# Kernel optimization log

Hardware: AMD Instinct MI355X
Metric: run time of the kernel (lower is better)

## Reference

```python
import jax, jax.numpy as jnp
import numpy as np

B, S, D, H, DK = 2, 2048, 1024, 16, 64  # d_model = n_heads * d_k

def setup_inputs() -> dict:
    key = jax.random.key(0)
    ks = jax.random.split(key, 11)
    s = 1.0 / np.sqrt(D)
    return {
        "Q": jax.random.normal(ks[0], (B, S, D), jnp.float32),
        "K": jax.random.normal(ks[1], (B, S, D), jnp.float32),
        "V": jax.random.normal(ks[2], (B, S, D), jnp.float32),
        "wq": jax.random.normal(ks[3], (D, D), jnp.float32) * s,
        "bq": jnp.zeros((D,), jnp.float32),
        "wk": jax.random.normal(ks[4], (D, D), jnp.float32) * s,
        "bk": jnp.zeros((D,), jnp.float32),
        "wv": jax.random.normal(ks[5], (D, D), jnp.float32) * s,
        "bv": jnp.zeros((D,), jnp.float32),
        "wo": jax.random.normal(ks[6], (D, D), jnp.float32) * s,
        "bo": jnp.zeros((D,), jnp.float32),
    }

def reference(Q, K, V, wq, bq, wk, bk, wv, bv, wo, bo):
    # linear projections (torch Linear: x @ W^T + b)
    q = Q @ wq.T + bq
    k = K @ wk.T + bk
    v = V @ wv.T + bv
    # split heads -> [B, H, S, DK]
    def split(t):
        return t.reshape(B, S, H, DK).transpose(0, 2, 1, 3)
    q, k, v = split(q), split(k), split(v)
    scale = 1.0 / np.sqrt(DK)
    scores = jnp.einsum('bhqd,bhkd->bhqk', q, k) * scale  # [B,H,S,S]
    probs = jax.nn.softmax(scores, axis=-1)
    # dropout is identity in eval mode
    ctx = jnp.einsum('bhqk,bhkd->bhqd', probs, v)  # [B,H,S,DK]
    ctx = ctx.transpose(0, 2, 1, 3).reshape(B, S, D)
    return ctx @ wo.T + bo
```

## Files before the change

kernel.cpp:

```cpp
#include <hip/hip_runtime.h>

#define S_LEN 2048
#define DMODEL 1024
#define DHEAD 64

typedef _Float16 half8 __attribute__((ext_vector_type(8)));
typedef _Float16 half4 __attribute__((ext_vector_type(4)));
typedef float f32x4 __attribute__((ext_vector_type(4)));

#define LOG2E 1.4426950408889634f

__device__ __forceinline__ void async_copy16(const void* g, void* l) {
  __builtin_amdgcn_global_load_lds((__attribute__((address_space(1))) const void*)g,
                                   (__attribute__((address_space(3))) void*)l,
                                   16, 0, 0);
}

__device__ __forceinline__ void stage16_cvt(const float* __restrict__ gp, _Float16* lp) {
  float4 f0 = ((const float4*)gp)[0];
  float4 f1 = ((const float4*)gp)[1];
  float4 f2 = ((const float4*)gp)[2];
  float4 f3 = ((const float4*)gp)[3];
  half8 h0, h1;
  h0[0] = (_Float16)f0.x; h0[1] = (_Float16)f0.y; h0[2] = (_Float16)f0.z; h0[3] = (_Float16)f0.w;
  h0[4] = (_Float16)f1.x; h0[5] = (_Float16)f1.y; h0[6] = (_Float16)f1.z; h0[7] = (_Float16)f1.w;
  h1[0] = (_Float16)f2.x; h1[1] = (_Float16)f2.y; h1[2] = (_Float16)f2.z; h1[3] = (_Float16)f2.w;
  h1[4] = (_Float16)f3.x; h1[5] = (_Float16)f3.y; h1[6] = (_Float16)f3.z; h1[7] = (_Float16)f3.w;
  *(half8*)lp = h0;
  *(half8*)(lp + 8) = h1;
}

__global__ __launch_bounds__(256) void convert_w(const float* __restrict__ wq,
                                                 const float* __restrict__ wk,
                                                 const float* __restrict__ wv,
                                                 _Float16* __restrict__ dst) {
  const float* src = (blockIdx.y == 0) ? wq : (blockIdx.y == 1) ? wk : wv;
  _Float16* d = dst + (size_t)blockIdx.y * (DMODEL * DMODEL);
  int i = (blockIdx.x * 256 + threadIdx.x) * 4;
  float4 v = *(const float4*)(src + i);
  half4 h;
  h[0] = (_Float16)v.x; h[1] = (_Float16)v.y;
  h[2] = (_Float16)v.z; h[3] = (_Float16)v.w;
  *(half4*)(d + i) = h;
}

__global__ __launch_bounds__(256) void convert_wo(const float* __restrict__ wo,
                                                  _Float16* __restrict__ dst) {
  int i = (blockIdx.x * 256 + threadIdx.x) * 4;
  float4 v = *(const float4*)(wo + i);
  half4 h;
  h[0] = (_Float16)v.x; h[1] = (_Float16)v.y;
  h[2] = (_Float16)v.z; h[3] = (_Float16)v.w;
  *(half4*)(dst + i) = h;
}

__global__ __launch_bounds__(256) void qkv_gemm(
    const float* __restrict__ Qf, const float* __restrict__ Kf, const float* __restrict__ Vf,
    const _Float16* __restrict__ wh,
    const float* __restrict__ bq, const float* __restrict__ bk, const float* __restrict__ bv,
    _Float16* __restrict__ qo, _Float16* __restrict__ ko, _Float16* __restrict__ vt) {
  __shared__ __align__(16) _Float16 As[128 * 32];
  __shared__ __align__(16) _Float16 Bs[128 * 32];
  const int tid = threadIdx.x;
  const int wave = tid >> 6, lane = tid & 63;
  const int m15 = lane & 15, quad = lane >> 4;
  const int m0 = blockIdx.x * 128;
  const int gn0 = blockIdx.y * 128;
  const int sel = gn0 >> 10;
  const int n0 = gn0 & 1023;
  const float* Ag = (sel == 0) ? Qf : (sel == 1) ? Kf : Vf;
  const _Float16* Wg = wh + (size_t)sel * (DMODEL * DMODEL);
  const float* bias = (sel == 0) ? bq : (sel == 1) ? bk : bv;

  const int wm = (wave & 1) * 64, wn = (wave >> 1) * 64;
  const int sr = tid >> 1, sc16 = (tid & 1) * 16;

  f32x4 acc[4][4];
#pragma unroll
  for (int i = 0; i < 4; i++)
#pragma unroll
    for (int j = 0; j < 4; j++) {
      f32x4 z = {0.f, 0.f, 0.f, 0.f};
      acc[i][j] = z;
    }

  for (int k0 = 0; k0 < DMODEL; k0 += 32) {
#pragma unroll
    for (int p = 0; p < 2; p++) {
      int e = p * 2048 + tid * 8;
      async_copy16(Wg + (size_t)(n0 + (e >> 5)) * DMODEL + k0 + (e & 31),
                   (char*)Bs + p * 4096 + wave * 1024);
    }
    stage16_cvt(Ag + (size_t)(m0 + sr) * DMODEL + k0 + sc16, &As[sr * 32 + sc16]);
    __syncthreads();
    half8 af[4], bf[4];
#pragma unroll
    for (int i = 0; i < 4; i++)
      af[i] = *(const half8*)&As[(wm + i * 16 + m15) * 32 + quad * 8];
#pragma unroll
    for (int j = 0; j < 4; j++)
      bf[j] = *(const half8*)&Bs[(wn + j * 16 + m15) * 32 + quad * 8];
#pragma unroll
    for (int i = 0; i < 4; i++)
#pragma unroll
      for (int j = 0; j < 4; j++)
        acc[i][j] = __builtin_amdgcn_mfma_f32_16x16x32_f16(af[i], bf[j], acc[i][j], 0, 0, 0);
    __syncthreads();
  }
  if (sel != 2) {
    _Float16* outp = (sel == 0) ? qo : ko;
    const float scale = (sel == 0) ? (0.125f * LOG2E) : 1.0f;
#pragma unroll
    for (int i = 0; i < 4; i++) {
#pragma unroll
      for (int j = 0; j < 4; j++) {
        int gn = n0 + wn + j * 16 + m15;
        float bb = bias[gn];
#pragma unroll
        for (int r = 0; r < 4; r++) {
          int gm = m0 + wm + i * 16 + quad * 4 + r;
          outp[(size_t)gm * DMODEL + gn] = (_Float16)((acc[i][j][r] + bb) * scale);
        }
      }
    }
  } else {
#pragma unroll
    for (int i = 0; i < 4; i++) {
      int gm0 = m0 + wm + i * 16 + quad * 4;
      int b = gm0 >> 11, s = gm0 & 2047;
#pragma unroll
      for (int j = 0; j < 4; j++) {
        int gn = n0 + wn + j * 16 + m15;
        int h = gn >> 6, dk = gn & 63;
        float bb = bias[gn];
        half4 hv;
        hv[0] = (_Float16)(acc[i][j][0] + bb);
        hv[1] = (_Float16)(acc[i][j][1] + bb);
        hv[2] = (_Float16)(acc[i][j][2] + bb);
        hv[3] = (_Float16)(acc[i][j][3] + bb);
        *(half4*)(vt + ((size_t)(b * 16 + h) * 64 + dk) * 2048 + s) = hv;
      }
    }
  }
}

__global__ __launch_bounds__(256) void attn_kernel(const _Float16* __restrict__ qh,
                                                   const _Float16* __restrict__ kh,
                                                   const _Float16* __restrict__ vt,
                                                   _Float16* __restrict__ ctx) {
  __shared__ __align__(16) _Float16 Ks[64 * 72];
  __shared__ __align__(16) _Float16 Vs[64 * 72];
  __shared__ __align__(16) _Float16 Pl[4][16 * 72];
  const int tid = threadIdx.x;
  const int wave = tid >> 6, lane = tid & 63;
  const int m15 = lane & 15, quad = lane >> 4;
  const int q0 = blockIdx.x * 64;
  const int h = blockIdx.y, b = blockIdx.z;
  const size_t base = (size_t)b * S_LEN * DMODEL + (size_t)h * DHEAD;
  const size_t vbase = (size_t)(b * 16 + h) * 64 * 2048;

  const int qrow = q0 + wave * 16 + m15;
  half8 qf0 = *(const half8*)(qh + base + (size_t)qrow * DMODEL + quad * 8);
  half8 qf1 = *(const half8*)(qh + base + (size_t)qrow * DMODEL + 32 + quad * 8);

  f32x4 O[4];
#pragma unroll
  for (int i = 0; i < 4; i++) { f32x4 z = {0.f, 0.f, 0.f, 0.f}; O[i] = z; }
  float lsum[4] = {0.f, 0.f, 0.f, 0.f};

  _Float16* Pw = &Pl[wave][0];
  const int srow = tid >> 3, scol = (tid & 7) * 8;

  for (int kv0 = 0; kv0 < S_LEN; kv0 += 64) {
    *(half8*)&Ks[srow * 72 + scol] =
        *(const half8*)(kh + base + (size_t)(kv0 + srow) * DMODEL + scol);
    *(half8*)&Ks[(srow + 32) * 72 + scol] =
        *(const half8*)(kh + base + (size_t)(kv0 + srow + 32) * DMODEL + scol);
    *(half8*)&Vs[srow * 72 + scol] =
        *(const half8*)(vt + vbase + (size_t)srow * S_LEN + kv0 + scol);
    *(half8*)&Vs[(srow + 32) * 72 + scol] =
        *(const half8*)(vt + vbase + (size_t)(srow + 32) * S_LEN + kv0 + scol);
    __syncthreads();

    f32x4 sc[4];
#pragma unroll
    for (int t = 0; t < 4; t++) {
      half8 kf0 = *(const half8*)&Ks[(t * 16 + m15) * 72 + quad * 8];
      half8 kf1 = *(const half8*)&Ks[(t * 16 + m15) * 72 + 32 + quad * 8];
      f32x4 z = {0.f, 0.f, 0.f, 0.f};
      sc[t] = __builtin_amdgcn_mfma_f32_16x16x32_f16(qf0, kf0, z, 0, 0, 0);
      sc[t] = __builtin_amdgcn_mfma_f32_16x16x32_f16(qf1, kf1, sc[t], 0, 0, 0);
    }

#pragma unroll
    for (int t = 0; t < 4; t++)
#pragma unroll
      for (int r = 0; r < 4; r++) {
        float p = exp2f(sc[t][r]);
        lsum[r] += p;
        Pw[(quad * 4 + r) * 72 + t * 16 + m15] = (_Float16)p;
      }

    half8 pf0 = *(const half8*)&Pw[m15 * 72 + quad * 8];
    half8 pf1 = *(const half8*)&Pw[m15 * 72 + 32 + quad * 8];

#pragma unroll
    for (int t = 0; t < 4; t++) {
      half8 vf0 = *(const half8*)&Vs[(t * 16 + m15) * 72 + quad * 8];
      half8 vf1 = *(const half8*)&Vs[(t * 16 + m15) * 72 + 32 + quad * 8];
      O[t] = __builtin_amdgcn_mfma_f32_16x16x32_f16(pf0, vf0, O[t], 0, 0, 0);
      O[t] = __builtin_amdgcn_mfma_f32_16x16x32_f16(pf1, vf1, O[t], 0, 0, 0);
    }
    __syncthreads();
  }

#pragma unroll
  for (int msk = 1; msk < 16; msk <<= 1)
#pragma unroll
    for (int r = 0; r < 4; r++) lsum[r] += __shfl_xor(lsum[r], msk);
  float inv[4];
#pragma unroll
  for (int r = 0; r < 4; r++) inv[r] = 1.0f / lsum[r];

#pragma unroll
  for (int t = 0; t < 4; t++)
#pragma unroll
    for (int r = 0; r < 4; r++) {
      int row = q0 + wave * 16 + quad * 4 + r;
      ctx[base + (size_t)row * DMODEL + t * 16 + m15] = (_Float16)(O[t][r] * inv[r]);
    }
}

__global__ __launch_bounds__(256) void out_gemm(const _Float16* __restrict__ ch,
                                                const _Float16* __restrict__ who,
                                                const float* __restrict__ bo,
                                                float* __restrict__ out) {
  __shared__ __align__(16) _Float16 As[128 * 32];
  __shared__ __align__(16) _Float16 Bs[128 * 32];
  const int tid = threadIdx.x;
  const int wave = tid >> 6, lane = tid & 63;
  const int m15 = lane & 15, quad = lane >> 4;
  const int m0 = blockIdx.x * 128, n0 = blockIdx.y * 128;
  const int wm = (wave & 1) * 64, wn = (wave >> 1) * 64;

  f32x4 acc[4][4];
#pragma unroll
  for (int i = 0; i < 4; i++)
#pragma unroll
    for (int j = 0; j < 4; j++) {
      f32x4 z = {0.f, 0.f, 0.f, 0.f};
      acc[i][j] = z;
    }

  for (int k0 = 0; k0 < DMODEL; k0 += 32) {
#pragma unroll
    for (int p = 0; p < 2; p++) {
      int e = p * 2048 + tid * 8;
      async_copy16(ch + (size_t)(m0 + (e >> 5)) * DMODEL + k0 + (e & 31),
                   (char*)As + p * 4096 + wave * 1024);
      async_copy16(who + (size_t)(n0 + (e >> 5)) * DMODEL + k0 + (e & 31),
                   (char*)Bs + p * 4096 + wave * 1024);
    }
    __syncthreads();
    half8 af[4], bf[4];
#pragma unroll
    for (int i = 0; i < 4; i++)
      af[i] = *(const half8*)&As[(wm + i * 16 + m15) * 32 + quad * 8];
#pragma unroll
    for (int j = 0; j < 4; j++)
      bf[j] = *(const half8*)&Bs[(wn + j * 16 + m15) * 32 + quad * 8];
#pragma unroll
    for (int i = 0; i < 4; i++)
#pragma unroll
      for (int j = 0; j < 4; j++)
        acc[i][j] = __builtin_amdgcn_mfma_f32_16x16x32_f16(af[i], bf[j], acc[i][j], 0, 0, 0);
    __syncthreads();
  }
#pragma unroll
  for (int i = 0; i < 4; i++) {
#pragma unroll
    for (int j = 0; j < 4; j++) {
      int gn = n0 + wn + j * 16 + m15;
      float bb = bo[gn];
#pragma unroll
      for (int r = 0; r < 4; r++) {
        int gm = m0 + wm + i * 16 + quad * 4 + r;
        out[(size_t)gm * DMODEL + gn] = acc[i][j][r] + bb;
      }
    }
  }
}

extern "C" void kernel_launch(void* const* d_in, const int* in_sizes, int n_in,
                              void* d_out, int out_size, void* d_ws, size_t ws_size,
                              hipStream_t stream) {
  (void)in_sizes; (void)n_in; (void)out_size; (void)ws_size;
  const float* Q  = (const float*)d_in[0];
  const float* K  = (const float*)d_in[1];
  const float* V  = (const float*)d_in[2];
  const float* wq = (const float*)d_in[3];
  const float* bq = (const float*)d_in[4];
  const float* wk = (const float*)d_in[5];
  const float* bk = (const float*)d_in[6];
  const float* wv = (const float*)d_in[7];
  const float* bv = (const float*)d_in[8];
  const float* wo = (const float*)d_in[9];
  const float* bo = (const float*)d_in[10];
  float* out = (float*)d_out;

  _Float16* qh = (_Float16*)d_out;
  _Float16* kh = qh + (size_t)4194304;
  _Float16* vt = (_Float16*)d_ws;
  _Float16* wh = vt + (size_t)4194304;
  _Float16* ch = vt + (size_t)4194304;
  _Float16* who = (_Float16*)d_ws;

  convert_w<<<dim3(1024, 3), 256, 0, stream>>>(wq, wk, wv, wh);
  qkv_gemm<<<dim3(32, 24), 256, 0, stream>>>(Q, K, V, wh, bq, bk, bv, qh, kh, vt);
  attn_kernel<<<dim3(32, 16, 2), 256, 0, stream>>>(qh, kh, vt, ch);
  convert_wo<<<dim3(1024), 256, 0, stream>>>(wo, who);
  out_gemm<<<dim3(32, 8), 256, 0, stream>>>(ch, who, bo, out);
}
```

Baseline: 270.5 us.

## Double-buffer attention K/V with async LDS loads and register-only P transpose

```diff
diff --git a/kernel.cpp b/kernel.cpp
--- a/kernel.cpp
+++ b/kernel.cpp
@@ -7,6 +7,7 @@
 typedef _Float16 half8 __attribute__((ext_vector_type(8)));
 typedef _Float16 half4 __attribute__((ext_vector_type(4)));
 typedef float f32x4 __attribute__((ext_vector_type(4)));
+typedef int i32x4 __attribute__((ext_vector_type(4)));
 
 #define LOG2E 1.4426950408889634f
 
@@ -148,87 +149,111 @@
                                                    const _Float16* __restrict__ kh,
                                                    const _Float16* __restrict__ vt,
                                                    _Float16* __restrict__ ctx) {
-  __shared__ __align__(16) _Float16 Ks[64 * 72];
-  __shared__ __align__(16) _Float16 Vs[64 * 72];
-  __shared__ __align__(16) _Float16 Pl[4][16 * 72];
+  __shared__ __align__(16) _Float16 Ks[2][64 * 64];
+  __shared__ __align__(16) _Float16 Vs[2][64 * 64];
   const int tid = threadIdx.x;
   const int wave = tid >> 6, lane = tid & 63;
-  const int m15 = lane & 15, quad = lane >> 4;
+  const int m15 = lane & 15, qd = lane >> 4;
   const int q0 = blockIdx.x * 64;
   const int h = blockIdx.y, b = blockIdx.z;
   const size_t base = (size_t)b * S_LEN * DMODEL + (size_t)h * DHEAD;
   const size_t vbase = (size_t)(b * 16 + h) * 64 * 2048;
 
   const int qrow = q0 + wave * 16 + m15;
-  half8 qf0 = *(const half8*)(qh + base + (size_t)qrow * DMODEL + quad * 8);
-  half8 qf1 = *(const half8*)(qh + base + (size_t)qrow * DMODEL + 32 + quad * 8);
-
-  f32x4 O[4];
-#pragma unroll
-  for (int i = 0; i < 4; i++) { f32x4 z = {0.f, 0.f, 0.f, 0.f}; O[i] = z; }
-  float lsum[4] = {0.f, 0.f, 0.f, 0.f};
-
-  _Float16* Pw = &Pl[wave][0];
-  const int srow = tid >> 3, scol = (tid & 7) * 8;
-
-  for (int kv0 = 0; kv0 < S_LEN; kv0 += 64) {
-    *(half8*)&Ks[srow * 72 + scol] =
-        *(const half8*)(kh + base + (size_t)(kv0 + srow) * DMODEL + scol);
-    *(half8*)&Ks[(srow + 32) * 72 + scol] =
-        *(const half8*)(kh + base + (size_t)(kv0 + srow + 32) * DMODEL + scol);
-    *(half8*)&Vs[srow * 72 + scol] =
-        *(const half8*)(vt + vbase + (size_t)srow * S_LEN + kv0 + scol);
-    *(half8*)&Vs[(srow + 32) * 72 + scol] =
-        *(const half8*)(vt + vbase + (size_t)(srow + 32) * S_LEN + kv0 + scol);
-    __syncthreads();
+  half8 qf0 = *(const half8*)(qh + base + (size_t)qrow * DMODEL + qd * 8);
+  half8 qf1 = *(const half8*)(qh + base + (size_t)qrow * DMODEL + 32 + qd * 8);
+
+  const int l8 = lane >> 3, s8 = lane & 7;
+  const int swz = (s8 ^ l8) * 8;
+  const _Float16* ksrc = kh + base + (size_t)(wave * 8 + l8) * DMODEL + swz;
+  const _Float16* vsrc = vt + vbase + (size_t)(wave * 8 + l8) * S_LEN + swz;
+  char* kdst = (char*)&Ks[0][0] + wave * 1024;
+  char* vdst = (char*)&Vs[0][0] + wave * 1024;
+
+  const int kcol0 = ((qd ^ (m15 & 7)) << 4);
+
+  f32x4 acc[4];
+#pragma unroll
+  for (int i = 0; i < 4; i++) { f32x4 z = {0.f, 0.f, 0.f, 0.f}; acc[i] = z; }
+  float lsum = 0.f;
+
+#pragma unroll
+  for (int p = 0; p < 2; p++) {
+    async_copy16(ksrc + (size_t)(p * 32) * DMODEL, kdst + p * 4096);
+    async_copy16(vsrc + (size_t)(p * 32) * S_LEN, vdst + p * 4096);
+  }
+  __syncthreads();
+
+  for (int it = 0; it < 32; it++) {
+    const int buf = it & 1;
+    if (it < 31) {
+      const int kv = (it + 1) * 64;
+#pragma unroll
+      for (int p = 0; p < 2; p++) {
+        async_copy16(ksrc + (size_t)(kv + p * 32) * DMODEL, kdst + (buf ^ 1) * 8192 + p * 4096);
+        async_copy16(vsrc + (size_t)(p * 32) * S_LEN + kv, vdst + (buf ^ 1) * 8192 + p * 4096);
+      }
+    }
+    const char* kb = (const char*)&Ks[buf][0];
+    const char* vb = (const char*)&Vs[buf][0];
 
     f32x4 sc[4];
 #pragma unroll
     for (int t = 0; t < 4; t++) {
-      half8 kf0 = *(const half8*)&Ks[(t * 16 + m15) * 72 + quad * 8];
-      half8 kf1 = *(const half8*)&Ks[(t * 16 + m15) * 72 + 32 + quad * 8];
+      half8 kf0 = *(const half8*)(kb + (t * 16 + m15) * 128 + kcol0);
+      half8 kf1 = *(const half8*)(kb + (t * 16 + m15) * 128 + (kcol0 ^ 64));
       f32x4 z = {0.f, 0.f, 0.f, 0.f};
-      sc[t] = __builtin_amdgcn_mfma_f32_16x16x32_f16(qf0, kf0, z, 0, 0, 0);
-      sc[t] = __builtin_amdgcn_mfma_f32_16x16x32_f16(qf1, kf1, sc[t], 0, 0, 0);
-    }
-
-#pragma unroll
-    for (int t = 0; t < 4; t++)
-#pragma unroll
-      for (int r = 0; r < 4; r++) {
-        float p = exp2f(sc[t][r]);
-        lsum[r] += p;
-        Pw[(quad * 4 + r) * 72 + t * 16 + m15] = (_Float16)p;
-      }
-
-    half8 pf0 = *(const half8*)&Pw[m15 * 72 + quad * 8];
-    half8 pf1 = *(const half8*)&Pw[m15 * 72 + 32 + quad * 8];
-
+      sc[t] = __builtin_amdgcn_mfma_f32_16x16x32_f16(kf0, qf0, z, 0, 0, 0);
+      sc[t] = __builtin_amdgcn_mfma_f32_16x16x32_f16(kf1, qf1, sc[t], 0, 0, 0);
+    }
+
+    int pk[4][2];
 #pragma unroll
     for (int t = 0; t < 4; t++) {
-      half8 vf0 = *(const half8*)&Vs[(t * 16 + m15) * 72 + quad * 8];
-      half8 vf1 = *(const half8*)&Vs[(t * 16 + m15) * 72 + 32 + quad * 8];
-      O[t] = __builtin_amdgcn_mfma_f32_16x16x32_f16(pf0, vf0, O[t], 0, 0, 0);
-      O[t] = __builtin_amdgcn_mfma_f32_16x16x32_f16(pf1, vf1, O[t], 0, 0, 0);
-    }
-    __syncthreads();
-  }
-
-#pragma unroll
-  for (int msk = 1; msk < 16; msk <<= 1)
-#pragma unroll
-    for (int r = 0; r < 4; r++) lsum[r] += __shfl_xor(lsum[r], msk);
-  float inv[4];
-#pragma unroll
-  for (int r = 0; r < 4; r++) inv[r] = 1.0f / lsum[r];
-
-#pragma unroll
-  for (int t = 0; t < 4; t++)
-#pragma unroll
-    for (int r = 0; r < 4; r++) {
-      int row = q0 + wave * 16 + quad * 4 + r;
-      ctx[base + (size_t)row * DMODEL + t * 16 + m15] = (_Float16)(O[t][r] * inv[r]);
-    }
+      float e0 = exp2f(sc[t][0]);
+      float e1 = exp2f(sc[t][1]);
+      float e2 = exp2f(sc[t][2]);
+      float e3 = exp2f(sc[t][3]);
+      lsum += (e0 + e1) + (e2 + e3);
+      pk[t][0] = __builtin_bit_cast(int, __builtin_amdgcn_cvt_pkrtz(e0, e1));
+      pk[t][1] = __builtin_bit_cast(int, __builtin_amdgcn_cvt_pkrtz(e2, e3));
+    }
+
+    i32x4 fh[2];
+#pragma unroll
+    for (int t1 = 0; t1 < 2; t1++) {
+#pragma unroll
+      for (int p = 0; p < 2; p++) {
+        auto s1 = __builtin_amdgcn_permlane32_swap(pk[2 * t1][p], pk[2 * t1 + 1][p], false, false);
+        auto s2 = __builtin_amdgcn_permlane16_swap(s1[0], s1[1], false, false);
+        fh[t1][p] = (int)s2[0];
+        fh[t1][2 + p] = (int)s2[1];
+      }
+    }
+    half8 pA = __builtin_bit_cast(half8, fh[0]);
+    half8 pB = __builtin_bit_cast(half8, fh[1]);
+
+#pragma unroll
+    for (int td = 0; td < 4; td++) {
+      half8 vf0 = *(const half8*)(vb + (td * 16 + m15) * 128 + kcol0);
+      half8 vf1 = *(const half8*)(vb + (td * 16 + m15) * 128 + (kcol0 ^ 64));
+      acc[td] = __builtin_amdgcn_mfma_f32_16x16x32_f16(vf0, pA, acc[td], 0, 0, 0);
+      acc[td] = __builtin_amdgcn_mfma_f32_16x16x32_f16(vf1, pB, acc[td], 0, 0, 0);
+    }
+    __syncthreads();
+  }
+
+  lsum += __shfl_xor(lsum, 16);
+  lsum += __shfl_xor(lsum, 32);
+  const float inv = 1.0f / lsum;
+
+#pragma unroll
+  for (int td = 0; td < 4; td++) {
+    half4 hv;
+#pragma unroll
+    for (int r = 0; r < 4; r++) hv[r] = (_Float16)(acc[td][r] * inv);
+    *(half4*)(ctx + base + (size_t)qrow * DMODEL + td * 16 + qd * 4) = hv;
+  }
 }
 
 __global__ __launch_bounds__(256) void out_gemm(const _Float16* __restrict__ ch,
```

New measurement: 258.8 us. -4.3%, faster.
